# Performance work log

Hardware: AMD Instinct MI355X
Metric: run time of the kernel (lower is better)

The kernel has to match this reference:

```python
import jax, jax.numpy as jnp
import numpy as np

EPS = 1e-7


def ciou_pairwise(b1, b2):
    # b1: (N,1,4), b2: (1,N,4) in xyxy; returns (N,N) CIoU
    b1x1, b1y1, b1x2, b1y2 = b1[..., 0], b1[..., 1], b1[..., 2], b1[..., 3]
    b2x1, b2y1, b2x2, b2y2 = b2[..., 0], b2[..., 1], b2[..., 2], b2[..., 3]

    # intersection
    iw = jnp.clip(jnp.minimum(b1x2, b2x2) - jnp.maximum(b1x1, b2x1), 0.0)
    ih = jnp.clip(jnp.minimum(b1y2, b2y2) - jnp.maximum(b1y1, b2y1), 0.0)
    inter = iw * ih

    w1, h1 = b1x2 - b1x1, b1y2 - b1y1
    w2, h2 = b2x2 - b2x1, b2y2 - b2y1
    union = w1 * h1 + w2 * h2 - inter + EPS
    iou = inter / union

    # smallest enclosing box diagonal
    cw = jnp.maximum(b1x2, b2x2) - jnp.minimum(b1x1, b2x1)
    ch = jnp.maximum(b1y2, b2y2) - jnp.minimum(b1y1, b2y1)
    c2 = cw * cw + ch * ch + EPS

    # squared center distance
    rho2 = ((b2x1 + b2x2 - b1x1 - b1x2) ** 2 + (b2y1 + b2y2 - b1y1 - b1y2) ** 2) / 4.0

    # aspect-ratio consistency term
    v = (4.0 / (np.pi ** 2)) * (jnp.arctan(w2 / (h2 + EPS)) - jnp.arctan(w1 / (h1 + EPS))) ** 2
    alpha = jax.lax.stop_gradient(v / (v - iou + (1.0 + EPS)))
    return iou - (rho2 / c2 + v * alpha)


def setup_inputs() -> dict:
    key = jax.random.key(0)
    k1, k2, k3 = jax.random.split(key, 3)
    N = 4096
    conf = jax.random.uniform(k1, (N, 1), dtype=jnp.float32)           # confidence in [0,1)
    xy1 = jax.random.uniform(k2, (N, 2), dtype=jnp.float32) * 600.0    # top-left corner
    wh = jax.random.uniform(k3, (N, 2), dtype=jnp.float32) * 100.0 + 1.0  # width/height >= 1
    x = jnp.concatenate([conf, xy1, xy1 + wh], axis=1)                 # (N, 5): conf, x1, y1, x2, y2
    gamma = jnp.zeros((1,), dtype=jnp.float32)
    return {"x": x, "gamma": gamma}


def reference(x, gamma):
    boxes = x[:, 1:]
    conf = x[:, 0]
    iou = ciou_pairwise(boxes[:, None, :], boxes[None, :, :])          # (N, N)
    conf_matrix = conf[:, None] * conf[None, :]                        # (N, N) outer product
    attention = jax.nn.softmax(iou * conf_matrix, axis=-1)             # (N, N)
    x_prime = x * gamma + attention @ x                                # (N, 5)
    return jax.nn.sigmoid(x_prime)
```

## Files before the change

kernel.cpp:

```cpp
#include <hip/hip_runtime.h>
#include <math.h>

#define N 4096
#define FEPS 1e-7f
#define BLK 256
#define JT 64
#define CH (N / JT)
#define LSTRIDE 12
#define N6 (N * 6)


__device__ __forceinline__ void box_record(const float* __restrict__ x, int i, float* rec) {
    float cf = x[i * 5 + 0], x1 = x[i * 5 + 1], y1 = x[i * 5 + 2];
    float x2 = x[i * 5 + 3], y2 = x[i * 5 + 4];
    float w = x2 - x1, h = y2 - y1;
    rec[0] = cf; rec[1] = x1; rec[2] = y1; rec[3] = x2; rec[4] = y2;
    rec[5] = (x1 + x2) * 0.5f; rec[6] = (y1 + y2) * 0.5f; rec[7] = w; rec[8] = h;
    rec[9] = w * h + 0.5f * FEPS;
    rec[10] = 0.6366197723675814f * atanf(w / (h + FEPS));
    rec[11] = cf * 1.2011224087864498f;
}

__global__ __launch_bounds__(BLK) void ciou_attn_kernel(
        const float* __restrict__ x,
        float* __restrict__ part) {
    __shared__ float jrec[CH * LSTRIDE];
    const int tid = threadIdx.x;
    const int gb = blockIdx.x / JT;
    const int jt = blockIdx.x % JT;
    const int i = gb * BLK + tid;

    if (tid < CH) box_record(x, jt * CH + tid, &jrec[tid * LSTRIDE]);

    float R[12];
    box_record(x, i, R);
    const float rx1 = R[1], ry1 = R[2], rx2 = R[3], ry2 = R[4];
    const float rhx = R[5], rhy = R[6], rw = R[7], rh = R[8];
    const float rareps = R[9], rat = R[10], rcf2 = R[11];

    __syncthreads();

    float sum = 0.f, a0 = 0.f, a1 = 0.f, a2 = 0.f, a3 = 0.f, a4 = 0.f;
    const float ONEP = 1.f + FEPS;

#pragma unroll 4
    for (int jj = 0; jj < CH; jj++) {
        const float* fj = &jrec[jj * LSTRIDE];
        float jcf = fj[0], jx1 = fj[1], jy1 = fj[2], jx2 = fj[3], jy2 = fj[4];
        float jhx = fj[5], jhy = fj[6], jw = fj[7], jh = fj[8];
        float jareps = fj[9], jat = fj[10], jcf2 = fj[11];

        float iwr = fminf(rx2, jx2) - fmaxf(rx1, jx1);
        float ihr = fminf(ry2, jy2) - fmaxf(ry1, jy1);
        float iw = fmaxf(iwr, 0.f);
        float ih = fmaxf(ihr, 0.f);
        float inter = iw * ih;
        float uni = (rareps + jareps) - inter;
        float iou = fminf(inter * __builtin_amdgcn_rcpf(uni), 1.0f);
        float cw = (rw + jw) - iwr;
        float ch = (rh + jh) - ihr;
        float c2 = fmaf(cw, cw, fmaf(ch, ch, FEPS));
        float dx = jhx - rhx;
        float dy = jhy - rhy;
        float rho2 = fmaf(dx, dx, dy * dy);
        float da = jat - rat;
        float v = da * da;
        float den = (v - iou) + ONEP;
        float valpha = (v * v) * __builtin_amdgcn_rcpf(den);
        float ciou = iou - fmaf(rho2, __builtin_amdgcn_rcpf(c2), valpha);
        float e = __builtin_amdgcn_exp2f(ciou * (rcf2 * jcf2));
        sum += e;
        a0 = fmaf(e, jcf, a0);
        a1 = fmaf(e, jx1, a1);
        a2 = fmaf(e, jy1, a2);
        a3 = fmaf(e, jx2, a3);
        a4 = fmaf(e, jy2, a4);
    }

    float* p = part + (size_t)jt * N6 + (size_t)i * 6;
    p[0] = sum; p[1] = a0; p[2] = a1; p[3] = a2; p[4] = a3; p[5] = a4;
}

__global__ void epilogue_kernel(const float* __restrict__ x,
                                const float* __restrict__ gamma,
                                const float* __restrict__ part,
                                float* __restrict__ out) {
    int idx = blockIdx.x * blockDim.x + threadIdx.x;
    if (idx >= N * 5) return;
    int i = idx / 5, c = idx % 5;
    float se = 0.f, a = 0.f;
    const float* p = part + (size_t)i * 6;
#pragma unroll 8
    for (int jt = 0; jt < JT; jt++) {
        se += p[jt * (size_t)N6 + 0];
        a  += p[jt * (size_t)N6 + 1 + c];
    }
    float xp = x[idx] * gamma[0] + a / se;
    out[idx] = 1.f / (1.f + expf(-xp));
}

extern "C" void kernel_launch(void* const* d_in, const int* in_sizes, int n_in,
                              void* d_out, int out_size, void* d_ws, size_t ws_size,
                              hipStream_t stream) {
    const float* x = (const float*)d_in[0];
    const float* gamma = (const float*)d_in[1];
    float* out = (float*)d_out;
    float* part = (float*)d_ws;

    ciou_attn_kernel<<<(N / BLK) * JT, BLK, 0, stream>>>(x, part);
    epilogue_kernel<<<(N * 5 + 255) / 256, 256, 0, stream>>>(x, gamma, part, out);
}
```

Measured before the change: 83.84 us.

## Register-block four rows per thread and pack shared j records as float4

Each thread now computes four i rows, so each shared-memory j record is read once per four pair evaluations, and the records are stored as three float4 values for vector LDS loads. The j dimension is split into 256 chunks instead of 64, which keeps the grid at 1024 blocks with 16 j per block. The epilogue now has to sum four times as many partials, and the per-thread register use is higher, which can lower occupancy.

```diff
diff --git a/kernel.cpp b/kernel.cpp
--- a/kernel.cpp
+++ b/kernel.cpp
@@ -4,81 +4,102 @@
 #define N 4096
 #define FEPS 1e-7f
 #define BLK 256
-#define JT 64
+#define R 4
+#define RPB (BLK * R)
+#define GB (N / RPB)
+#define JT 256
 #define CH (N / JT)
-#define LSTRIDE 12
 #define N6 (N * 6)
 
-
-__device__ __forceinline__ void box_record(const float* __restrict__ x, int i, float* rec) {
-    float cf = x[i * 5 + 0], x1 = x[i * 5 + 1], y1 = x[i * 5 + 2];
-    float x2 = x[i * 5 + 3], y2 = x[i * 5 + 4];
-    float w = x2 - x1, h = y2 - y1;
-    rec[0] = cf; rec[1] = x1; rec[2] = y1; rec[3] = x2; rec[4] = y2;
-    rec[5] = (x1 + x2) * 0.5f; rec[6] = (y1 + y2) * 0.5f; rec[7] = w; rec[8] = h;
-    rec[9] = w * h + 0.5f * FEPS;
-    rec[10] = 0.6366197723675814f * atanf(w / (h + FEPS));
-    rec[11] = cf * 1.2011224087864498f;
-}
 
 __global__ __launch_bounds__(BLK) void ciou_attn_kernel(
         const float* __restrict__ x,
         float* __restrict__ part) {
-    __shared__ float jrec[CH * LSTRIDE];
+    __shared__ float4 jv[CH * 3];
     const int tid = threadIdx.x;
     const int gb = blockIdx.x / JT;
     const int jt = blockIdx.x % JT;
-    const int i = gb * BLK + tid;
 
-    if (tid < CH) box_record(x, jt * CH + tid, &jrec[tid * LSTRIDE]);
+    if (tid < CH) {
+        int j = jt * CH + tid;
+        const float* xj = x + (size_t)j * 5;
+        float cf = xj[0], x1 = xj[1], y1 = xj[2], x2 = xj[3], y2 = xj[4];
+        float w = x2 - x1, h = y2 - y1;
+        jv[tid * 3 + 0] = make_float4(cf, x1, y1, x2);
+        jv[tid * 3 + 1] = make_float4(y2, (x1 + x2) * 0.5f, (y1 + y2) * 0.5f, w);
+        jv[tid * 3 + 2] = make_float4(h, w * h + 0.5f * FEPS,
+                                      0.6366197723675814f * atanf(w / (h + FEPS)),
+                                      cf * 1.2011224087864498f);
+    }
 
-    float R[12];
-    box_record(x, i, R);
-    const float rx1 = R[1], ry1 = R[2], rx2 = R[3], ry2 = R[4];
-    const float rhx = R[5], rhy = R[6], rw = R[7], rh = R[8];
-    const float rareps = R[9], rat = R[10], rcf2 = R[11];
+    float rx1[R], ry1[R], rx2[R], ry2[R], rhx[R], rhy[R];
+    float rw[R], rh[R], rareps[R], rat[R], rcf2[R];
+#pragma unroll
+    for (int r = 0; r < R; r++) {
+        int i = gb * RPB + r * BLK + tid;
+        const float* xi = x + (size_t)i * 5;
+        float cf = xi[0], x1 = xi[1], y1 = xi[2], x2 = xi[3], y2 = xi[4];
+        float w = x2 - x1, h = y2 - y1;
+        rx1[r] = x1; ry1[r] = y1; rx2[r] = x2; ry2[r] = y2;
+        rhx[r] = (x1 + x2) * 0.5f; rhy[r] = (y1 + y2) * 0.5f;
+        rw[r] = w; rh[r] = h;
+        rareps[r] = w * h + 0.5f * FEPS;
+        rat[r] = 0.6366197723675814f * atanf(w / (h + FEPS));
+        rcf2[r] = cf * 1.2011224087864498f;
+    }
 
     __syncthreads();
 
-    float sum = 0.f, a0 = 0.f, a1 = 0.f, a2 = 0.f, a3 = 0.f, a4 = 0.f;
+    float sum[R], a0[R], a1[R], a2[R], a3[R], a4[R];
+#pragma unroll
+    for (int r = 0; r < R; r++) {
+        sum[r] = 0.f; a0[r] = 0.f; a1[r] = 0.f; a2[r] = 0.f; a3[r] = 0.f; a4[r] = 0.f;
+    }
     const float ONEP = 1.f + FEPS;
 
-#pragma unroll 4
+#pragma unroll 2
     for (int jj = 0; jj < CH; jj++) {
-        const float* fj = &jrec[jj * LSTRIDE];
-        float jcf = fj[0], jx1 = fj[1], jy1 = fj[2], jx2 = fj[3], jy2 = fj[4];
-        float jhx = fj[5], jhy = fj[6], jw = fj[7], jh = fj[8];
-        float jareps = fj[9], jat = fj[10], jcf2 = fj[11];
-
-        float iwr = fminf(rx2, jx2) - fmaxf(rx1, jx1);
-        float ihr = fminf(ry2, jy2) - fmaxf(ry1, jy1);
-        float iw = fmaxf(iwr, 0.f);
-        float ih = fmaxf(ihr, 0.f);
-        float inter = iw * ih;
-        float uni = (rareps + jareps) - inter;
-        float iou = fminf(inter * __builtin_amdgcn_rcpf(uni), 1.0f);
-        float cw = (rw + jw) - iwr;
-        float ch = (rh + jh) - ihr;
-        float c2 = fmaf(cw, cw, fmaf(ch, ch, FEPS));
-        float dx = jhx - rhx;
-        float dy = jhy - rhy;
-        float rho2 = fmaf(dx, dx, dy * dy);
-        float da = jat - rat;
-        float v = da * da;
-        float den = (v - iou) + ONEP;
-        float valpha = (v * v) * __builtin_amdgcn_rcpf(den);
-        float ciou = iou - fmaf(rho2, __builtin_amdgcn_rcpf(c2), valpha);
-        float e = __builtin_amdgcn_exp2f(ciou * (rcf2 * jcf2));
-        sum += e;
-        a0 = fmaf(e, jcf, a0);
-        a1 = fmaf(e, jx1, a1);
-        a2 = fmaf(e, jy1, a2);
-        a3 = fmaf(e, jx2, a3);
-        a4 = fmaf(e, jy2, a4);
+        float4 A = jv[jj * 3 + 0], B = jv[jj * 3 + 1], C = jv[jj * 3 + 2];
+        float jcf = A.x, jx1 = A.y, jy1 = A.z, jx2 = A.w;
+        float jy2 = B.x, jhx = B.y, jhy = B.z, jw = B.w;
+        float jh = C.x, jareps = C.y, jat = C.z, jcf2 = C.w;
+#pragma unroll
+        for (int r = 0; r < R; r++) {
+            float iwr = fminf(rx2[r], jx2) - fmaxf(rx1[r], jx1);
+            float ihr = fminf(ry2[r], jy2) - fmaxf(ry1[r], jy1);
+            float iw = fmaxf(iwr, 0.f);
+            float ih = fmaxf(ihr, 0.f);
+            float inter = iw * ih;
+            float uni = (rareps[r] + jareps) - inter;
+            float iou = fminf(inter * __builtin_amdgcn_rcpf(uni), 1.0f);
+            float cw = (rw[r] + jw) - iwr;
+            float chh = (rh[r] + jh) - ihr;
+            float c2 = fmaf(cw, cw, fmaf(chh, chh, FEPS));
+            float dx = jhx - rhx[r];
+            float dy = jhy - rhy[r];
+            float rho2 = fmaf(dx, dx, dy * dy);
+            float da = jat - rat[r];
+            float v = da * da;
+            float den = (v - iou) + ONEP;
+            float valpha = (v * v) * __builtin_amdgcn_rcpf(den);
+            float ciou = iou - fmaf(rho2, __builtin_amdgcn_rcpf(c2), valpha);
+            float e = __builtin_amdgcn_exp2f(ciou * (rcf2[r] * jcf2));
+            sum[r] += e;
+            a0[r] = fmaf(e, jcf, a0[r]);
+            a1[r] = fmaf(e, jx1, a1[r]);
+            a2[r] = fmaf(e, jy1, a2[r]);
+            a3[r] = fmaf(e, jx2, a3[r]);
+            a4[r] = fmaf(e, jy2, a4[r]);
+        }
     }
 
-    float* p = part + (size_t)jt * N6 + (size_t)i * 6;
-    p[0] = sum; p[1] = a0; p[2] = a1; p[3] = a2; p[4] = a3; p[5] = a4;
+#pragma unroll
+    for (int r = 0; r < R; r++) {
+        int i = gb * RPB + r * BLK + tid;
+        float* p = part + (size_t)jt * N6 + (size_t)i * 6;
+        p[0] = sum[r]; p[1] = a0[r]; p[2] = a1[r];
+        p[3] = a2[r]; p[4] = a3[r]; p[5] = a4[r];
+    }
 }
 
 __global__ void epilogue_kernel(const float* __restrict__ x,
@@ -107,6 +128,6 @@
     float* out = (float*)d_out;
     float* part = (float*)d_ws;
 
-    ciou_attn_kernel<<<(N / BLK) * JT, BLK, 0, stream>>>(x, part);
+    ciou_attn_kernel<<<GB * JT, BLK, 0, stream>>>(x, part);
     epilogue_kernel<<<(N * 5 + 255) / 256, 256, 0, stream>>>(x, gamma, part, out);
 }
```

Result: slower. 108.3 us (+29.2%).
